# Optimization experiments

Measured on AMD Instinct MI355X. Metric: run time of the kernel, lower is better.

## Reference

```python
import jax, jax.numpy as jnp
import numpy as np

B, T, D, H, STRIDE, MLP = 2, 2048, 1024, 16, 8, 4096
HD = D // H
EPS = 1e-5


def _ln(x, g, b):
    m = x.mean(-1, keepdims=True)
    v = x.var(-1, keepdims=True)
    return (x - m) * jax.lax.rsqrt(v + EPS) * g + b


def setup_inputs() -> dict:
    key = jax.random.key(0)
    ks = jax.random.split(key, 6)
    s = lambda k, shape: (jax.random.normal(k, shape, jnp.float32) * 0.02)
    return {
        "x": jax.random.normal(ks[0], (B, T, D), jnp.float32),
        "w_in": s(ks[1], (3 * D, D)),   # torch in_proj_weight
        "b_in": jnp.zeros((3 * D,), jnp.float32),
        "w_out": s(ks[2], (D, D)),      # attn out_proj
        "b_out": jnp.zeros((D,), jnp.float32),
        "w1": s(ks[3], (MLP, D)),       # mlp first Linear (torch layout [out,in])
        "b1": jnp.zeros((MLP,), jnp.float32),
        "w2": s(ks[4], (D, MLP)),       # mlp second Linear
        "b2": jnp.zeros((D,), jnp.float32),
        "ln1_g": jnp.ones((D,), jnp.float32),
        "ln1_b": jnp.zeros((D,), jnp.float32),
        "ln2_g": jnp.ones((D,), jnp.float32),
        "ln2_b": jnp.zeros((D,), jnp.float32),
    }


def reference(x, w_in, b_in, w_out, b_out, w1, b1, w2, b2,
              ln1_g, ln1_b, ln2_g, ln2_b):
    Bs, Ts, Ds = x.shape
    xn = _ln(x, ln1_g, ln1_b)
    # fused qkv projection (torch Linear: y = x @ W.T + b)
    qkv = xn @ w_in.T + b_in                              # [B,T,3D]
    q, k, v = jnp.split(qkv, 3, axis=-1)
    to_heads = lambda t: t.reshape(Bs, Ts, H, HD).transpose(0, 2, 1, 3)
    q, k, v = to_heads(q), to_heads(k), to_heads(v)       # [B,H,T,hd]
    scores = jnp.einsum("bhqd,bhkd->bhqk", q, k) / jnp.sqrt(jnp.float32(HD))
    # mask: rows at multiples of STRIDE attend everywhere; others only to self
    idx = jnp.arange(Ts)
    allowed = ((idx % STRIDE) == 0)[:, None] | (idx[:, None] == idx[None, :])
    scores = jnp.where(allowed, scores, -jnp.inf)
    attn = jax.nn.softmax(scores, axis=-1)
    o = jnp.einsum("bhqk,bhkd->bhqd", attn, v)            # [B,H,T,hd]
    o = o.transpose(0, 2, 1, 3).reshape(Bs, Ts, Ds)
    o = o @ w_out.T + b_out
    x = x + o
    xn = _ln(x, ln2_g, ln2_b)
    h = jax.nn.gelu(xn @ w1.T + b1, approximate=False)    # torch nn.GELU default = exact
    x = x + (h @ w2.T + b2)
    return x
```

## Files before the change

### kernel.cpp

```cpp
#include <hip/hip_runtime.h>

#define D_ 1024
#define T_ 2048
#define B_ 2
#define H_ 16
#define MLP_ 4096
#define NTOK (B_*T_)
#define QG 256
#define L2E 1.44269504088896340736f

typedef float f32x4 __attribute__((ext_vector_type(4)));
typedef __bf16 bf16x8 __attribute__((ext_vector_type(8)));

__device__ __forceinline__ unsigned short f2bf(float f) {
  unsigned int u = __float_as_uint(f);
  u += 0x7fff + ((u >> 16) & 1);
  return (unsigned short)(u >> 16);
}

__device__ __forceinline__ float wave_sum(float v) {
  for (int o = 32; o > 0; o >>= 1) v += __shfl_down(v, o, 64);
  return v;
}

__device__ __forceinline__ void gload16(const unsigned short* g, unsigned short* l) {
  __builtin_amdgcn_global_load_lds(
      (const __attribute__((address_space(1))) void*)g,
      (__attribute__((address_space(3))) void*)l, 16, 0, 0);
}

__device__ __forceinline__ unsigned ldsoff(const void* p) {
  return (unsigned)(size_t)(const __attribute__((address_space(3))) void*)p;
}

__device__ __forceinline__ void agload16(const unsigned short* g, unsigned m0v) {
  unsigned su = __builtin_amdgcn_readfirstlane(m0v);
  asm volatile("s_mov_b32 m0, %0\n\t"
               "global_load_lds_dwordx4 %1, off"
               :: "s"(su), "v"(g) : "memory");
}

#define N4_WIN  786432
#define N4_WOUT 262144
#define N4_W1   1048576
#define N4_W2   1048576
#define NCASTB  12288
__global__ void castln_kernel(const float* __restrict__ w_in,
                              const float* __restrict__ w_out,
                              const float* __restrict__ w1,
                              const float* __restrict__ w2,
                              unsigned short* __restrict__ o_in,
                              unsigned short* __restrict__ o_out,
                              unsigned short* __restrict__ o1,
                              unsigned short* __restrict__ o2,
                              const float* __restrict__ x,
                              const float* __restrict__ g,
                              const float* __restrict__ b,
                              unsigned short* __restrict__ xn) {
  int blk = blockIdx.x;
  int tid = threadIdx.x;
  if (blk < NTOK) {
    int wave = tid >> 6, lane = tid & 63;
    float4 v = ((const float4*)(x + (size_t)blk * D_))[tid];
    float s  = v.x + v.y + v.z + v.w;
    float s2 = v.x*v.x + v.y*v.y + v.z*v.z + v.w*v.w;
    s = wave_sum(s); s2 = wave_sum(s2);
    __shared__ float r1[4], r2[4];
    if (lane == 0) { r1[wave] = s; r2[wave] = s2; }
    __syncthreads();
    float ts  = r1[0] + r1[1] + r1[2] + r1[3];
    float ts2 = r2[0] + r2[1] + r2[2] + r2[3];
    float mean = ts * (1.0f / D_);
    float var  = ts2 * (1.0f / D_) - mean * mean;
    float rs = rsqrtf(var + 1e-5f);
    float4 gv = ((const float4*)g)[tid];
    float4 bv = ((const float4*)b)[tid];
    ushort4 o;
    o.x = f2bf((v.x - mean) * rs * gv.x + bv.x);
    o.y = f2bf((v.y - mean) * rs * gv.y + bv.y);
    o.z = f2bf((v.z - mean) * rs * gv.z + bv.z);
    o.w = f2bf((v.w - mean) * rs * gv.w + bv.w);
    ((ushort4*)(xn + (size_t)blk * D_))[tid] = o;
  } else {
    int i = (blk - NTOK) * 256 + tid;
    const float* src; unsigned short* dst; int j = i;
    if (i < N4_WIN) { src = w_in; dst = o_in; }
    else if ((j -= N4_WIN) < N4_WOUT) { src = w_out; dst = o_out; }
    else if ((j -= N4_WOUT) < N4_W1) { src = w1; dst = o1; }
    else { j -= N4_W1; src = w2; dst = o2; }
    float4 v = ((const float4*)src)[j];
    ushort4 o;
    o.x = f2bf(v.x); o.y = f2bf(v.y); o.z = f2bf(v.z); o.w = f2bf(v.w);
    ((ushort4*)dst)[j] = o;
  }
}

__global__ void reduce_ln_kernel(const float* __restrict__ part,
                                 const float* __restrict__ x,
                                 const float* __restrict__ bias,
                                 const float* __restrict__ g,
                                 const float* __restrict__ b,
                                 float* __restrict__ x1,
                                 unsigned short* __restrict__ xn2) {
  int row = blockIdx.x;
  int tid = threadIdx.x;
  int wave = tid >> 6, lane = tid & 63;
  size_t base = (size_t)row * (D_ / 4) + tid;
  float4 v = ((const float4*)x)[base];
  float4 bo = ((const float4*)bias)[tid];
  v.x += bo.x; v.y += bo.y; v.z += bo.z; v.w += bo.w;
#pragma unroll
  for (int c = 0; c < 2; ++c) {
    float4 p = ((const float4*)part)[(size_t)c * (NTOK * (D_ / 4)) + base];
    v.x += p.x; v.y += p.y; v.z += p.z; v.w += p.w;
  }
  ((float4*)x1)[base] = v;
  float s  = v.x + v.y + v.z + v.w;
  float s2 = v.x*v.x + v.y*v.y + v.z*v.z + v.w*v.w;
  s = wave_sum(s); s2 = wave_sum(s2);
  __shared__ float r1[4], r2[4];
  if (lane == 0) { r1[wave] = s; r2[wave] = s2; }
  __syncthreads();
  float ts  = r1[0] + r1[1] + r1[2] + r1[3];
  float ts2 = r2[0] + r2[1] + r2[2] + r2[3];
  float mean = ts * (1.0f / D_);
  float var  = ts2 * (1.0f / D_) - mean * mean;
  float rs = rsqrtf(var + 1e-5f);
  float4 gv = ((const float4*)g)[tid];
  float4 bv = ((const float4*)b)[tid];
  ushort4 o;
  o.x = f2bf((v.x - mean) * rs * gv.x + bv.x);
  o.y = f2bf((v.y - mean) * rs * gv.y + bv.y);
  o.z = f2bf((v.z - mean) * rs * gv.z + bv.z);
  o.w = f2bf((v.w - mean) * rs * gv.w + bv.w);
  ((ushort4*)xn2)[base] = o;
}

__global__ void reduce_out_kernel(const float* __restrict__ part,
                                  const float* __restrict__ x1,
                                  const float* __restrict__ bias,
                                  float* __restrict__ out) {
  int i = blockIdx.x * 256 + threadIdx.x;
  float4 v = ((const float4*)x1)[i];
  float4 bo = ((const float4*)bias)[i & (D_ / 4 - 1)];
  v.x += bo.x; v.y += bo.y; v.z += bo.z; v.w += bo.w;
#pragma unroll
  for (int c = 0; c < 2; ++c) {
    float4 p = ((const float4*)part)[(size_t)c * (NTOK * (D_ / 4)) + i];
    v.x += p.x; v.y += p.y; v.z += p.z; v.w += p.w;
  }
  ((float4*)out)[i] = v;
}

template<int EPI>
__global__ __launch_bounds__(256)
void gemm128p_kernel(const unsigned short* __restrict__ A, int LDA,
                     const unsigned short* __restrict__ Bm, int LDB,
                     void* __restrict__ Cv, size_t sC, int LDC,
                     const float* __restrict__ bias,
                     int K, int nx, int ny) {
  __shared__ __align__(16) unsigned short As[2 * 8192];
  __shared__ __align__(16) unsigned short Bs[2 * 8192];
  const int flat = blockIdx.x;
  const int sxc = nx >> 1;
  const int nSuper = sxc * (ny >> 2);
  int s = flat % nSuper, pos = flat / nSuper;
  int sx = s % sxc, sy = s / sxc;
  const int bx = sx * 2 + (pos & 1);
  const int by = sy * 4 + (pos >> 1);
  const int m0 = by * 128, n0 = bx * 128;
  const int kOff = blockIdx.z * K;
  const int tid = threadIdx.x;
  const int lane = tid & 63, wave = tid >> 6;
  const int wm = (wave >> 1) * 64, wn = (wave & 1) * 64;
  const int fr = lane & 15, q = lane >> 4;
  const int f0 = ((q)     ^ (fr & 7)) << 3;
  const int f1 = ((4 + q) ^ (fr & 7)) << 3;

  const unsigned short* aS[4];
  const unsigned short* bS[4];
#pragma unroll
  for (int p = 0; p < 4; ++p) {
    int l = p * 256 + tid;
    int r = l >> 3;
    int cg = (l & 7) ^ (r & 7);
    aS[p] = A  + (size_t)(m0 + r) * LDA + kOff + cg * 8;
    bS[p] = Bm + (size_t)(n0 + r) * LDB + kOff + cg * 8;
  }
  const int NT = K >> 6;

  const unsigned aW = ldsoff(As) + wave * 1024;
  const unsigned bW = ldsoff(Bs) + wave * 1024;

#pragma unroll
  for (int p = 0; p < 4; ++p) {
    agload16(aS[p], aW + p * 4096);
    agload16(bS[p], bW + p * 4096);
  }
#pragma unroll
  for (int p = 0; p < 4; ++p) {
    agload16(aS[p] + 64, aW + 16384 + p * 4096);
    agload16(bS[p] + 64, bW + 16384 + p * 4096);
  }
  asm volatile("s_waitcnt vmcnt(8)");
  __builtin_amdgcn_sched_barrier(0);
  __builtin_amdgcn_s_barrier();

  f32x4 acc[4][4] = {};
  for (int t = 0; t < NT; ++t) {
    const int cb = (t & 1) << 13;
    const unsigned cbB = (t & 1) << 14;
    const unsigned short* Ab = As + cb;
    const unsigned short* Bb = Bs + cb;
    const int ko2 = (t + 2) << 6;
    {
      bf16x8 af[4], bfr[4];
#pragma unroll
      for (int i = 0; i < 4; ++i) af[i]  = *(const bf16x8*)&Ab[(wm + i * 16 + fr) * 64 + f0];
#pragma unroll
      for (int j = 0; j < 4; ++j) bfr[j] = *(const bf16x8*)&Bb[(wn + j * 16 + fr) * 64 + f0];
#pragma unroll
      for (int i = 0; i < 4; ++i)
#pragma unroll
        for (int j = 0; j < 4; ++j)
          acc[i][j] = __builtin_amdgcn_mfma_f32_16x16x32_bf16(af[i], bfr[j], acc[i][j], 0, 0, 0);
    }
    {
      bf16x8 af[4], bfr[4];
#pragma unroll
      for (int i = 0; i < 4; ++i) af[i]  = *(const bf16x8*)&Ab[(wm + i * 16 + fr) * 64 + f1];
#pragma unroll
      for (int j = 0; j < 4; ++j) bfr[j] = *(const bf16x8*)&Bb[(wn + j * 16 + fr) * 64 + f1];
#pragma unroll
      for (int i = 0; i < 4; ++i)
#pragma unroll
        for (int j = 0; j < 4; ++j)
          acc[i][j] = __builtin_amdgcn_mfma_f32_16x16x32_bf16(af[i], bfr[j], acc[i][j], 0, 0, 0);
    }
    __builtin_amdgcn_s_barrier();
    if (t + 2 < NT) {
#pragma unroll
      for (int p = 0; p < 4; ++p) {
        agload16(aS[p] + ko2, aW + cbB + p * 4096);
        agload16(bS[p] + ko2, bW + cbB + p * 4096);
      }
    }
    if (t + 1 < NT) {
      if (t + 2 < NT) asm volatile("s_waitcnt vmcnt(8)");
      else            asm volatile("s_waitcnt vmcnt(0)");
      __builtin_amdgcn_sched_barrier(0);
    }
    __builtin_amdgcn_s_barrier();
  }

  const int col = lane & 15, rbase = (lane >> 4) * 4;
#pragma unroll
  for (int i = 0; i < 4; ++i) {
#pragma unroll
    for (int j = 0; j < 4; ++j) {
      int gn = n0 + wn + j * 16 + col;
      int gmb = m0 + wm + i * 16 + rbase;
      float bv = (EPI == 2) ? bias[gn] : 0.0f;
#pragma unroll
      for (int r = 0; r < 4; ++r) {
        int gm = gmb + r;
        float v = acc[i][j][r] + bv;
        if (EPI == 2) {
          float u = v * (1.5957691216f + 0.0713548162f * v * v);
          float gl = v / (1.0f + exp2f(-L2E * u));
          ((unsigned short*)Cv)[(size_t)gm * LDC + gn] = f2bf(gl);
        } else {
          ((float*)Cv)[(size_t)blockIdx.z * sC + (size_t)gm * LDC + gn] = v;
        }
      }
    }
  }
}

template<int EPI>
__global__ __launch_bounds__(512)
void gemm256a_kernel(const unsigned short* __restrict__ A, int LDA,
                     const unsigned short* __restrict__ Bm, int LDB,
                     void* __restrict__ Cv, size_t sC, int LDC,
                     const float* __restrict__ bias,
                     int K, int nx) {
  __shared__ __align__(16) unsigned short As[2 * 16384];
  __shared__ __align__(16) unsigned short Bs[2 * 16384];
  const int tid = threadIdx.x;
  const int lane = tid & 63, w = tid >> 6;
  const int wm = w >> 2, wn = w & 3;
  const int fr = lane & 15, q = lane >> 4, xr = fr & 7;

  const int nwg = gridDim.x;
  const int bid = blockIdx.x;
  const int l = (bid & 7) * (nwg >> 3) + (bid >> 3);
  const int bx = l % nx, by = l / nx;
  const int m0 = by * 256, n0 = bx * 256;
  const int kOff = blockIdx.z * K;

  const unsigned short* aS[4];
  const unsigned short* bS[4];
#pragma unroll
  for (int s = 0; s < 4; ++s) {
    int ls = s * 512 + tid;
    int r = ls >> 3;
    int cg = (ls & 7) ^ (r & 7);
    aS[s] = A  + (size_t)(m0 + r) * LDA + kOff + cg * 8;
    bS[s] = Bm + (size_t)(n0 + r) * LDB + kOff + cg * 8;
  }
  const int NT = K >> 6;

  const unsigned asb = ldsoff(As), bsb = ldsoff(Bs);
  const unsigned aW = asb + w * 1024, bW = bsb + w * 1024;

#pragma unroll
  for (int s = 0; s < 4; ++s) {
    agload16(aS[s], aW + s * 8192);
    agload16(bS[s], bW + s * 8192);
  }
#pragma unroll
  for (int s = 0; s < 4; ++s) {
    agload16(aS[s] + 64, aW + 32768 + s * 8192);
    agload16(bS[s] + 64, bW + 32768 + s * 8192);
  }
  asm volatile("s_waitcnt vmcnt(8)");
  __builtin_amdgcn_sched_barrier(0);
  __builtin_amdgcn_s_barrier();

  const int aOff = ((wm * 128 + fr) << 7) + ((q ^ xr) << 4);
  const int bOff = ((wn * 64 + fr) << 7) + ((q ^ xr) << 4);

  f32x4 acc[8][4] = {};

  for (int t = 0; t < NT; ++t) {
    const int cb = (t & 1) << 15;
    const char* Ab = (const char*)As + cb;
    const char* Bb = (const char*)Bs + cb;
    const unsigned aWc = aW + cb, bWc = bW + cb;
    const int ko2 = (t + 2) << 6;
    bf16x8 af[2][4], bfr[2][4];

#pragma unroll
    for (int i = 0; i < 4; ++i) {
      af[0][i] = *(const bf16x8*)(Ab + aOff + i * 2048);
      af[1][i] = *(const bf16x8*)(Ab + (aOff ^ 64) + i * 2048);
    }
#pragma unroll
    for (int j = 0; j < 2; ++j) {
      bfr[0][j] = *(const bf16x8*)(Bb + bOff + j * 2048);
      bfr[1][j] = *(const bf16x8*)(Bb + (bOff ^ 64) + j * 2048);
    }
    __builtin_amdgcn_s_barrier();
    __builtin_amdgcn_s_setprio(1);
#pragma unroll
    for (int i = 0; i < 4; ++i)
#pragma unroll
      for (int j = 0; j < 2; ++j) {
        acc[i][j] = __builtin_amdgcn_mfma_f32_16x16x32_bf16(af[0][i], bfr[0][j], acc[i][j], 0, 0, 0);
        acc[i][j] = __builtin_amdgcn_mfma_f32_16x16x32_bf16(af[1][i], bfr[1][j], acc[i][j], 0, 0, 0);
      }
    __builtin_amdgcn_s_setprio(0);
    __builtin_amdgcn_s_barrier();

#pragma unroll
    for (int j = 2; j < 4; ++j) {
      bfr[0][j] = *(const bf16x8*)(Bb + bOff + j * 2048);
      bfr[1][j] = *(const bf16x8*)(Bb + (bOff ^ 64) + j * 2048);
    }
    if (t + 2 < NT) {
      agload16(aS[0] + ko2, aWc);
      agload16(aS[2] + ko2, aWc + 16384);
    }
    __builtin_amdgcn_s_barrier();
    __builtin_amdgcn_s_setprio(1);
#pragma unroll
    for (int i = 0; i < 4; ++i)
#pragma unroll
      for (int j = 0; j < 2; ++j) {
        acc[i][2 + j] = __builtin_amdgcn_mfma_f32_16x16x32_bf16(af[0][i], bfr[0][2 + j], acc[i][2 + j], 0, 0, 0);
        acc[i][2 + j] = __builtin_amdgcn_mfma_f32_16x16x32_bf16(af[1][i], bfr[1][2 + j], acc[i][2 + j], 0, 0, 0);
      }
    __builtin_amdgcn_s_setprio(0);
    __builtin_amdgcn_s_barrier();

#pragma unroll
    for (int i = 0; i < 4; ++i) {
      af[0][i] = *(const bf16x8*)(Ab + (aOff + 8192) + i * 2048);
      af[1][i] = *(const bf16x8*)(Ab + ((aOff + 8192) ^ 64) + i * 2048);
    }
    if (t + 2 < NT) {
      agload16(bS[0] + ko2, bWc);
      agload16(bS[1] + ko2, bWc + 8192);
      agload16(bS[2] + ko2, bWc + 16384);
      agload16(bS[3] + ko2, bWc + 24576);
    }
    __builtin_amdgcn_s_barrier();
    __builtin_amdgcn_s_setprio(1);
#pragma unroll
    for (int i = 0; i < 4; ++i)
#pragma unroll
      for (int j = 0; j < 2; ++j) {
        acc[4 + i][j] = __builtin_amdgcn_mfma_f32_16x16x32_bf16(af[0][i], bfr[0][j], acc[4 + i][j], 0, 0, 0);
        acc[4 + i][j] = __builtin_amdgcn_mfma_f32_16x16x32_bf16(af[1][i], bfr[1][j], acc[4 + i][j], 0, 0, 0);
      }
    __builtin_amdgcn_s_setprio(0);
    __builtin_amdgcn_s_barrier();

    if (t + 2 < NT) {
      agload16(aS[1] + ko2, aWc + 8192);
      agload16(aS[3] + ko2, aWc + 24576);
    }
    if (t + 1 < NT) {
      if (t + 2 < NT) asm volatile("s_waitcnt vmcnt(8)");
      else            asm volatile("s_waitcnt vmcnt(0)");
      __builtin_amdgcn_sched_barrier(0);
    }
    __builtin_amdgcn_s_barrier();
    __builtin_amdgcn_s_setprio(1);
#pragma unroll
    for (int i = 0; i < 4; ++i)
#pragma unroll
      for (int j = 0; j < 2; ++j) {
        acc[4 + i][2 + j] = __builtin_amdgcn_mfma_f32_16x16x32_bf16(af[0][i], bfr[0][2 + j], acc[4 + i][2 + j], 0, 0, 0);
        acc[4 + i][2 + j] = __builtin_amdgcn_mfma_f32_16x16x32_bf16(af[1][i], bfr[1][2 + j], acc[4 + i][2 + j], 0, 0, 0);
      }
    __builtin_amdgcn_s_setprio(0);
    __builtin_amdgcn_s_barrier();
  }

  const int col = lane & 15, rbase = (lane >> 4) * 4;
  const int gm0 = m0 + wm * 128 + rbase;
  const int gn0 = n0 + wn * 64 + col;
#pragma unroll
  for (int mi = 0; mi < 8; ++mi) {
#pragma unroll
    for (int j = 0; j < 4; ++j) {
      int gn = gn0 + j * 16;
      float bv = (EPI == 2) ? bias[gn] : 0.0f;
#pragma unroll
      for (int r = 0; r < 4; ++r) {
        int gm = gm0 + mi * 16 + r;
        float v = acc[mi][j][r] + bv;
        if (EPI == 2) {
          float u = v * (1.5957691216f + 0.0713548162f * v * v);
          float gl = v / (1.0f + exp2f(-L2E * u));
          ((unsigned short*)Cv)[(size_t)gm * LDC + gn] = f2bf(gl);
        } else {
          ((float*)Cv)[(size_t)blockIdx.z * sC + (size_t)gm * LDC + gn] = v;
        }
      }
    }
  }
}

template<int EPI>
__global__ __launch_bounds__(512)
void gemm256b_kernel(const unsigned short* __restrict__ A, int LDA,
                     const unsigned short* __restrict__ Bm, int LDB,
                     unsigned short* __restrict__ Cv, int LDC,
                     const float* __restrict__ bias,
                     unsigned short* __restrict__ aux1,
                     unsigned short* __restrict__ aux2,
                     int K, int nx) {
  __shared__ __align__(16) unsigned short As[2 * 4096];
  __shared__ __align__(16) unsigned short Bs[2 * 8192];
  const int tid = threadIdx.x;
  const int lane = tid & 63, wv = tid >> 6;
  const int wm = (wv >> 2) * 64, wn = (wv & 3) * 64;
  const int fr = lane & 15, q = lane >> 4;

  const int nwg = gridDim.x;
  const int bid = blockIdx.x;
  const int l = (bid & 7) * (nwg >> 3) + (bid >> 3);
  const int bx = l % nx, by = l / nx;
  const int m0 = by * 128, n0 = bx * 256;

  const int rA = tid >> 2, sA = tid & 3;
  const int cA = sA ^ ((rA >> 1) & 3);
  const unsigned short* aSrc = A  + (size_t)(m0 + rA) * LDA + cA * 8;
  const unsigned short* bSrc0 = Bm + (size_t)(n0 + rA) * LDB + cA * 8;
  const unsigned short* bSrc1 = Bm + (size_t)(n0 + 128 + rA) * LDB + cA * 8;
  const int NT = K >> 5;

  const unsigned aWb = ldsoff(As) + wv * 1024;
  const unsigned bWb = ldsoff(Bs) + wv * 1024;

  agload16(aSrc, aWb);
  agload16(bSrc0, bWb);
  agload16(bSrc1, bWb + 8192);
  agload16(aSrc + 32, aWb + 8192);
  agload16(bSrc0 + 32, bWb + 16384);
  agload16(bSrc1 + 32, bWb + 24576);
  asm volatile("s_waitcnt vmcnt(3)");
  __builtin_amdgcn_sched_barrier(0);
  __builtin_amdgcn_s_barrier();

  f32x4 acc[4][4] = {};
  for (int t = 0; t < NT; ++t) {
    const unsigned cbA = (t & 1) ? 8192u : 0u;
    const unsigned cbB = (t & 1) ? 16384u : 0u;
    const char* Ab = (const char*)As + cbA;
    const char* Bb = (const char*)Bs + cbB;
    const int ko2 = (t + 2) << 5;
    bf16x8 af[4], bfr[4];
#pragma unroll
    for (int i = 0; i < 4; ++i) {
      int ra = wm + i * 16 + fr;
      af[i] = *(const bf16x8*)(Ab + ra * 64 + ((q ^ ((ra >> 1) & 3)) << 4));
    }
#pragma unroll
    for (int j = 0; j < 4; ++j) {
      int rb = wn + j * 16 + fr;
      bfr[j] = *(const bf16x8*)(Bb + rb * 64 + ((q ^ ((rb >> 1) & 3)) << 4));
    }
#pragma unroll
    for (int i = 0; i < 4; ++i)
#pragma unroll
      for (int j = 0; j < 4; ++j)
        acc[i][j] = __builtin_amdgcn_mfma_f32_16x16x32_bf16(af[i], bfr[j], acc[i][j], 0, 0, 0);
    __builtin_amdgcn_s_barrier();
    if (t + 2 < NT) {
      agload16(aSrc + ko2, aWb + cbA);
      agload16(bSrc0 + ko2, bWb + cbB);
      agload16(bSrc1 + ko2, bWb + cbB + 8192);
    }
    if (t + 1 < NT) {
      if (t + 2 < NT) asm volatile("s_waitcnt vmcnt(3)");
      else            asm volatile("s_waitcnt vmcnt(0)");
      __builtin_amdgcn_sched_barrier(0);
    }
    __builtin_amdgcn_s_barrier();
  }

  const int col = lane & 15, rbase = (lane >> 4) * 4;
#pragma unroll
  for (int i = 0; i < 4; ++i) {
#pragma unroll
    for (int j = 0; j < 4; ++j) {
      int gn = n0 + wn + j * 16 + col;
      int gmb = m0 + wm + i * 16 + rbase;
      float bv = bias[gn];
#pragma unroll
      for (int r = 0; r < 4; ++r) {
        int gm = gmb + r;
        float v = acc[i][j][r] + bv;
        if (EPI == 2) {
          float u = v * (1.5957691216f + 0.0713548162f * v * v);
          float gl = v / (1.0f + exp2f(-L2E * u));
          Cv[(size_t)gm * LDC + gn] = f2bf(gl);
        } else {
          int sec = gn >> 10;
          int hh = (gn >> 6) & (H_ - 1);
          int dd = gn & 63;
          int t = gm & (T_ - 1);
          int b = gm >> 11;
          unsigned short bf = f2bf(v);
          if (sec == 0) {
            if (!(t & 7))
              aux1[(((size_t)(b * H_ + hh)) * QG + (t >> 3)) * 64 + dd] = bf;
          } else if (sec == 1) {
            aux2[(((size_t)(b * H_ + hh)) * T_ + t) * 64 + dd] = bf;
          } else {
            Cv[(size_t)gm * D_ + (gn - 2 * D_)] = bf;
          }
        }
      }
    }
  }
}

__global__ void vtrans_kernel(const unsigned short* __restrict__ vcomp,
                              unsigned short* __restrict__ Vt) {
  int blk = blockIdx.x;
  int tchunk = blk & 31;
  int bh = blk >> 5;
  int h = bh & (H_ - 1), b = bh >> 4;
  int t0 = tchunk * 64;
  __shared__ unsigned short ls[64][66];
  int tid = threadIdx.x;
#pragma unroll
  for (int it = 0; it < 16; ++it) {
    int linear = it * 256 + tid;
    int d = linear & 63, tl = linear >> 6;
    ls[d][tl] = vcomp[((size_t)(b * T_ + t0 + tl)) * D_ + h * 64 + d];
  }
  __syncthreads();
#pragma unroll
  for (int it = 0; it < 16; ++it) {
    int linear = it * 256 + tid;
    int tl = linear & 63, d = linear >> 6;
    Vt[((size_t)(bh * 64 + d)) * T_ + t0 + tl] = ls[d][tl];
  }
}

__global__ __launch_bounds__(256)
void flash_kernel(const unsigned short* __restrict__ Qg,
                  const unsigned short* __restrict__ Kh,
                  const unsigned short* __restrict__ Vt,
                  float* __restrict__ Opart,
                  float* __restrict__ ml) {
  const int kc = blockIdx.x, qt = blockIdx.y, bh = blockIdx.z;
  const int tid = threadIdx.x;
  const int lane = tid & 63, w = tid >> 6;
  const int fr = lane & 15, quad = lane >> 4;

  __shared__ __align__(16) unsigned short Qs[64 * 64];
  __shared__ __align__(16) unsigned short Ks[128 * 64];
  __shared__ __align__(16) unsigned short Vs[64 * 128];
  __shared__ __align__(16) unsigned short Ps[4 * 16 * 128];

  const unsigned short* Qbase = Qg + ((size_t)bh * 256 + qt * 64) * 64;
#pragma unroll
  for (int p = 0; p < 2; ++p) {
    int linear = p * 256 + tid;
    int r = linear >> 3, c = linear & 7;
    gload16(Qbase + r * 64 + (c ^ (r & 7)) * 8, &Qs[linear * 8]);
  }

  float m_run[4], l_run[4];
  f32x4 O[4] = {};
#pragma unroll
  for (int r = 0; r < 4; ++r) { m_run[r] = -3.0e38f; l_run[r] = 0.f; }

  const unsigned short* Kc = Kh + ((size_t)bh * T_ + kc * 512) * 64;
  const unsigned short* Vc = Vt + (size_t)bh * 64 * T_ + kc * 512;
  unsigned short* Pw = &Ps[w * 2048];
  const int arow = w * 16 + fr;

  for (int kt = 0; kt < 4; ++kt) {
    __syncthreads();
#pragma unroll
    for (int p = 0; p < 4; ++p) {
      int linear = p * 256 + tid;
      int r = linear >> 3, c = linear & 7;
      gload16(Kc + (size_t)(kt * 128 + r) * 64 + (c ^ (r & 7)) * 8, &Ks[linear * 8]);
    }
#pragma unroll
    for (int p = 0; p < 4; ++p) {
      int linear = p * 256 + tid;
      int r = linear >> 4, c = linear & 15;
      gload16(Vc + (size_t)r * T_ + kt * 128 + (c ^ (r & 7)) * 8, &Vs[linear * 8]);
    }
    __syncthreads();

    f32x4 s[8] = {};
    bf16x8 aq[2];
#pragma unroll
    for (int ks = 0; ks < 2; ++ks)
      aq[ks] = *(const bf16x8*)&Qs[arow * 64 + ((ks * 4 + quad) ^ (fr & 7)) * 8];
#pragma unroll
    for (int nf = 0; nf < 8; ++nf) {
      int krow = nf * 16 + fr;
#pragma unroll
      for (int ks = 0; ks < 2; ++ks) {
        bf16x8 bk = *(const bf16x8*)&Ks[krow * 64 + ((ks * 4 + quad) ^ (fr & 7)) * 8];
        s[nf] = __builtin_amdgcn_mfma_f32_16x16x32_bf16(aq[ks], bk, s[nf], 0, 0, 0);
      }
    }
    float alpha[4], rowsum[4];
#pragma unroll
    for (int r = 0; r < 4; ++r) {
      float mt = -3.0e38f;
#pragma unroll
      for (int nf = 0; nf < 8; ++nf) { s[nf][r] *= 0.125f; mt = fmaxf(mt, s[nf][r]); }
#pragma unroll
      for (int x = 1; x < 16; x <<= 1) mt = fmaxf(mt, __shfl_xor(mt, x, 64));
      float mn = fmaxf(m_run[r], mt);
      alpha[r] = exp2f((m_run[r] - mn) * L2E);
      m_run[r] = mn;
      rowsum[r] = 0.f;
    }
#pragma unroll
    for (int nf = 0; nf < 8; ++nf)
#pragma unroll
      for (int r = 0; r < 4; ++r) {
        float p = exp2f((s[nf][r] - m_run[r]) * L2E);
        s[nf][r] = p; rowsum[r] += p;
      }
#pragma unroll
    for (int r = 0; r < 4; ++r) {
#pragma unroll
      for (int x = 1; x < 16; x <<= 1) rowsum[r] += __shfl_xor(rowsum[r], x, 64);
      l_run[r] = l_run[r] * alpha[r] + rowsum[r];
    }
#pragma unroll
    for (int nf = 0; nf < 8; ++nf)
#pragma unroll
      for (int r = 0; r < 4; ++r) {
        int m = quad * 4 + r;
        int c = nf * 2 + (fr >> 3);
        Pw[m * 128 + ((c ^ (m & 7)) * 8) + (fr & 7)] = f2bf(s[nf][r]);
      }
#pragma unroll
    for (int nf2 = 0; nf2 < 4; ++nf2)
#pragma unroll
      for (int r = 0; r < 4; ++r) O[nf2][r] *= alpha[r];
#pragma unroll
    for (int ks2 = 0; ks2 < 4; ++ks2) {
      bf16x8 ap = *(const bf16x8*)&Pw[fr * 128 + (((ks2 * 4 + quad) ^ (fr & 7)) * 8)];
#pragma unroll
      for (int nf2 = 0; nf2 < 4; ++nf2) {
        int vrow = nf2 * 16 + fr;
        bf16x8 bv = *(const bf16x8*)&Vs[vrow * 128 + (((ks2 * 4 + quad) ^ (fr & 7)) * 8)];
        O[nf2] = __builtin_amdgcn_mfma_f32_16x16x32_bf16(ap, bv, O[nf2], 0, 0, 0);
      }
    }
  }

  int qbase = qt * 64 + w * 16;
  float* Ob = Opart + (((size_t)bh * 4 + kc) * 256 + qbase) * 64;
#pragma unroll
  for (int nf2 = 0; nf2 < 4; ++nf2)
#pragma unroll
    for (int r = 0; r < 4; ++r)
      Ob[(size_t)(quad * 4 + r) * 64 + nf2 * 16 + fr] = O[nf2][r];
  if (fr == 0) {
#pragma unroll
    for (int r = 0; r < 4; ++r) {
      size_t mi = ((((size_t)bh * 4 + kc) * 256) + qbase + quad * 4 + r) * 2;
      ml[mi] = m_run[r]; ml[mi + 1] = l_run[r];
    }
  }
}

__global__ void combine_kernel(const float* __restrict__ Opart,
                               const float* __restrict__ ml,
                               unsigned short* __restrict__ vcomp) {
  int idx = blockIdx.x * 256 + threadIdx.x;
  int c = idx & (D_ - 1);
  int qi = (idx >> 10) & (QG - 1);
  int b = idx >> 18;
  int h = c >> 6, d = c & 63;
  int bh = b * H_ + h;
  float m[4], l[4];
  float M = -3.0e38f;
#pragma unroll
  for (int ch = 0; ch < 4; ++ch) {
    size_t r = ((size_t)bh * 4 + ch) * 256 + qi;
    m[ch] = ml[r * 2]; l[ch] = ml[r * 2 + 1];
    M = fmaxf(M, m[ch]);
  }
  float osum = 0.f, lsum = 0.f;
#pragma unroll
  for (int ch = 0; ch < 4; ++ch) {
    size_t r = ((size_t)bh * 4 + ch) * 256 + qi;
    float wgt = exp2f((m[ch] - M) * L2E);
    osum += wgt * Opart[r * 64 + d];
    lsum += wgt * l[ch];
  }
  vcomp[((size_t)(b * T_ + qi * 8)) * D_ + c] = f2bf(osum / lsum);
}

extern "C" void kernel_launch(void* const* d_in, const int* in_sizes, int n_in,
                              void* d_out, int out_size, void* d_ws, size_t ws_size,
                              hipStream_t stream) {
  const float* x     = (const float*)d_in[0];
  const float* w_in  = (const float*)d_in[1];
  const float* b_in  = (const float*)d_in[2];
  const float* w_out = (const float*)d_in[3];
  const float* b_out = (const float*)d_in[4];
  const float* w1    = (const float*)d_in[5];
  const float* b1    = (const float*)d_in[6];
  const float* w2    = (const float*)d_in[7];
  const float* b2    = (const float*)d_in[8];
  const float* ln1_g = (const float*)d_in[9];
  const float* ln1_b = (const float*)d_in[10];
  const float* ln2_g = (const float*)d_in[11];
  const float* ln2_b = (const float*)d_in[12];
  float* out = (float*)d_out;

  char* ws = (char*)d_ws;
  size_t off = 0;
  auto alloc = [&](size_t bytes) -> void* {
    void* p = ws + off;
    off += (bytes + 255) & ~(size_t)255;
    return p;
  };
  unsigned short* w_inb = (unsigned short*)alloc((size_t)3 * D_ * D_ * 2);
  unsigned short* w_outb= (unsigned short*)alloc((size_t)D_ * D_ * 2);
  unsigned short* w1b   = (unsigned short*)alloc((size_t)MLP_ * D_ * 2);
  unsigned short* w2b   = (unsigned short*)alloc((size_t)D_ * MLP_ * 2);
  unsigned short* vcomp = (unsigned short*)alloc((size_t)NTOK * D_ * 2);
  float*          x1    = (float*)         alloc((size_t)NTOK * D_ * 4);
  unsigned short* xn2   = (unsigned short*)alloc((size_t)NTOK * D_ * 2);
  unsigned short* h     = (unsigned short*)alloc((size_t)NTOK * MLP_ * 2);
  char* U = (char*)alloc((size_t)40 * 1024 * 1024);
  float*          P2    = (float*)U;
  unsigned short* xn    = (unsigned short*)U;
  unsigned short* Qg    = (unsigned short*)(U + 8388608);
  unsigned short* Kh    = (unsigned short*)(U + 12582912);
  unsigned short* Vt    = (unsigned short*)(U + 20971520);
  float*          Opart = (float*)         (U + 29360128);
  float*          mlbuf = (float*)         (U + 37748736);

  castln_kernel<<<NTOK + NCASTB, 256, 0, stream>>>(
      w_in, w_out, w1, w2, w_inb, w_outb, w1b, w2b, x, ln1_g, ln1_b, xn);

  gemm256b_kernel<8><<<dim3(384, 1, 1), 512, 0, stream>>>(
      xn, D_, w_inb, D_, vcomp, 3 * D_, b_in, Qg, Kh, 1024, 12);

  vtrans_kernel<<<1024, 256, 0, stream>>>(vcomp, Vt);

  flash_kernel<<<dim3(4, 4, 32), 256, 0, stream>>>(Qg, Kh, Vt, Opart, mlbuf);

  combine_kernel<<<2048, 256, 0, stream>>>(Opart, mlbuf, vcomp);

  gemm128p_kernel<7><<<dim3(8 * 32, 1, 2), 256, 0, stream>>>(
      vcomp, D_, w_outb, D_, P2, (size_t)NTOK * D_, D_, nullptr,
      512, 8, 32);

  reduce_ln_kernel<<<NTOK, 256, 0, stream>>>(P2, x, b_out, ln2_g, ln2_b, x1, xn2);

  gemm256a_kernel<2><<<dim3(256, 1, 1), 512, 0, stream>>>(
      xn2, D_, w1b, D_, h, 0, MLP_, b1, 1024, 16);

  gemm128p_kernel<7><<<dim3(8 * 32, 1, 2), 256, 0, stream>>>(
      h, MLP_, w2b, MLP_, P2, (size_t)NTOK * D_, D_, nullptr,
      2048, 8, 32);

  reduce_out_kernel<<<4096, 256, 0, stream>>>(P2, x1, b2, out);
}
```

Measured before the change: 314.2 us.

## Replace split-K GEMMs with 64x128 tile GEMM fusing bias and residual

The out-projection and MLP-down GEMMs no longer use split-K with two partial fp32 buffers followed by separate reduction kernels. They now use a 64x128 tile GEMM over the full K dimension, with 512 blocks in an XCD-interleaved order, and add bias and residual directly in the epilogue. This removes the partial-sum writes and reads and the extra reduce launch. The cost is longer K loops per block, since the MLP-down GEMM now runs all 4096 of K in one block, and lower arithmetic intensity per tile.

```diff
diff --git a/kernel.cpp b/kernel.cpp
--- a/kernel.cpp
+++ b/kernel.cpp
@@ -95,26 +95,12 @@
   }
 }
 
-__global__ void reduce_ln_kernel(const float* __restrict__ part,
-                                 const float* __restrict__ x,
-                                 const float* __restrict__ bias,
-                                 const float* __restrict__ g,
-                                 const float* __restrict__ b,
-                                 float* __restrict__ x1,
-                                 unsigned short* __restrict__ xn2) {
+__global__ void ln_kernel(const float* __restrict__ x, const float* __restrict__ g,
+                          const float* __restrict__ b, unsigned short* __restrict__ out) {
   int row = blockIdx.x;
   int tid = threadIdx.x;
   int wave = tid >> 6, lane = tid & 63;
-  size_t base = (size_t)row * (D_ / 4) + tid;
-  float4 v = ((const float4*)x)[base];
-  float4 bo = ((const float4*)bias)[tid];
-  v.x += bo.x; v.y += bo.y; v.z += bo.z; v.w += bo.w;
-#pragma unroll
-  for (int c = 0; c < 2; ++c) {
-    float4 p = ((const float4*)part)[(size_t)c * (NTOK * (D_ / 4)) + base];
-    v.x += p.x; v.y += p.y; v.z += p.z; v.w += p.w;
-  }
-  ((float4*)x1)[base] = v;
+  float4 v = ((const float4*)(x + (size_t)row * D_))[tid];
   float s  = v.x + v.y + v.z + v.w;
   float s2 = v.x*v.x + v.y*v.y + v.z*v.z + v.w*v.w;
   s = wave_sum(s); s2 = wave_sum(s2);
@@ -133,59 +119,46 @@
   o.y = f2bf((v.y - mean) * rs * gv.y + bv.y);
   o.z = f2bf((v.z - mean) * rs * gv.z + bv.z);
   o.w = f2bf((v.w - mean) * rs * gv.w + bv.w);
-  ((ushort4*)xn2)[base] = o;
-}
-
-__global__ void reduce_out_kernel(const float* __restrict__ part,
-                                  const float* __restrict__ x1,
-                                  const float* __restrict__ bias,
-                                  float* __restrict__ out) {
-  int i = blockIdx.x * 256 + threadIdx.x;
-  float4 v = ((const float4*)x1)[i];
-  float4 bo = ((const float4*)bias)[i & (D_ / 4 - 1)];
-  v.x += bo.x; v.y += bo.y; v.z += bo.z; v.w += bo.w;
-#pragma unroll
-  for (int c = 0; c < 2; ++c) {
-    float4 p = ((const float4*)part)[(size_t)c * (NTOK * (D_ / 4)) + i];
-    v.x += p.x; v.y += p.y; v.z += p.z; v.w += p.w;
-  }
-  ((float4*)out)[i] = v;
-}
-
-template<int EPI>
+  ((ushort4*)(out + (size_t)row * D_))[tid] = o;
+}
+
 __global__ __launch_bounds__(256)
-void gemm128p_kernel(const unsigned short* __restrict__ A, int LDA,
-                     const unsigned short* __restrict__ Bm, int LDB,
-                     void* __restrict__ Cv, size_t sC, int LDC,
-                     const float* __restrict__ bias,
-                     int K, int nx, int ny) {
-  __shared__ __align__(16) unsigned short As[2 * 8192];
+void gemm64p_kernel(const unsigned short* __restrict__ A, int LDA,
+                    const unsigned short* __restrict__ Bm, int LDB,
+                    float* __restrict__ C,
+                    const float* __restrict__ bias,
+                    const float* __restrict__ xres,
+                    int K, int nx) {
+  __shared__ __align__(16) unsigned short As[2 * 4096];
   __shared__ __align__(16) unsigned short Bs[2 * 8192];
-  const int flat = blockIdx.x;
-  const int sxc = nx >> 1;
-  const int nSuper = sxc * (ny >> 2);
-  int s = flat % nSuper, pos = flat / nSuper;
-  int sx = s % sxc, sy = s / sxc;
-  const int bx = sx * 2 + (pos & 1);
-  const int by = sy * 4 + (pos >> 1);
-  const int m0 = by * 128, n0 = bx * 128;
-  const int kOff = blockIdx.z * K;
   const int tid = threadIdx.x;
   const int lane = tid & 63, wave = tid >> 6;
-  const int wm = (wave >> 1) * 64, wn = (wave & 1) * 64;
+  const int wm = (wave >> 1) * 32, wn = (wave & 1) * 64;
   const int fr = lane & 15, q = lane >> 4;
   const int f0 = ((q)     ^ (fr & 7)) << 3;
   const int f1 = ((4 + q) ^ (fr & 7)) << 3;
 
-  const unsigned short* aS[4];
+  const int nwg = gridDim.x;
+  const int bid = blockIdx.x;
+  const int l = (bid & 7) * (nwg >> 3) + (bid >> 3);
+  const int bx = l % nx, by = l / nx;
+  const int m0 = by * 64, n0 = bx * 128;
+
+  const unsigned short* aS[2];
   const unsigned short* bS[4];
 #pragma unroll
+  for (int p = 0; p < 2; ++p) {
+    int ls = p * 256 + tid;
+    int r = ls >> 3;
+    int cg = (ls & 7) ^ (r & 7);
+    aS[p] = A + (size_t)(m0 + r) * LDA + cg * 8;
+  }
+#pragma unroll
   for (int p = 0; p < 4; ++p) {
-    int l = p * 256 + tid;
-    int r = l >> 3;
-    int cg = (l & 7) ^ (r & 7);
-    aS[p] = A  + (size_t)(m0 + r) * LDA + kOff + cg * 8;
-    bS[p] = Bm + (size_t)(n0 + r) * LDB + kOff + cg * 8;
+    int ls = p * 256 + tid;
+    int r = ls >> 3;
+    int cg = (ls & 7) ^ (r & 7);
+    bS[p] = Bm + (size_t)(n0 + r) * LDB + cg * 8;
   }
   const int NT = K >> 6;
 
@@ -193,46 +166,46 @@
   const unsigned bW = ldsoff(Bs) + wave * 1024;
 
 #pragma unroll
-  for (int p = 0; p < 4; ++p) {
-    agload16(aS[p], aW + p * 4096);
-    agload16(bS[p], bW + p * 4096);
-  }
-#pragma unroll
-  for (int p = 0; p < 4; ++p) {
-    agload16(aS[p] + 64, aW + 16384 + p * 4096);
-    agload16(bS[p] + 64, bW + 16384 + p * 4096);
-  }
-  asm volatile("s_waitcnt vmcnt(8)");
+  for (int p = 0; p < 2; ++p) agload16(aS[p], aW + p * 4096);
+#pragma unroll
+  for (int p = 0; p < 4; ++p) agload16(bS[p], bW + p * 4096);
+#pragma unroll
+  for (int p = 0; p < 2; ++p) agload16(aS[p] + 64, aW + 8192 + p * 4096);
+#pragma unroll
+  for (int p = 0; p < 4; ++p) agload16(bS[p] + 64, bW + 16384 + p * 4096);
+  asm volatile("s_waitcnt vmcnt(6)");
   __builtin_amdgcn_sched_barrier(0);
   __builtin_amdgcn_s_barrier();
 
-  f32x4 acc[4][4] = {};
+  f32x4 acc[2][4] = {};
   for (int t = 0; t < NT; ++t) {
-    const int cb = (t & 1) << 13;
-    const unsigned cbB = (t & 1) << 14;
-    const unsigned short* Ab = As + cb;
-    const unsigned short* Bb = Bs + cb;
+    const int cbA = (t & 1) << 12;
+    const int cbB = (t & 1) << 13;
+    const unsigned cbAB = (t & 1) << 13;
+    const unsigned cbBB = (t & 1) << 14;
+    const unsigned short* Ab = As + cbA;
+    const unsigned short* Bb = Bs + cbB;
     const int ko2 = (t + 2) << 6;
     {
-      bf16x8 af[4], bfr[4];
-#pragma unroll
-      for (int i = 0; i < 4; ++i) af[i]  = *(const bf16x8*)&Ab[(wm + i * 16 + fr) * 64 + f0];
+      bf16x8 af[2], bfr[4];
+#pragma unroll
+      for (int i = 0; i < 2; ++i) af[i]  = *(const bf16x8*)&Ab[(wm + i * 16 + fr) * 64 + f0];
 #pragma unroll
       for (int j = 0; j < 4; ++j) bfr[j] = *(const bf16x8*)&Bb[(wn + j * 16 + fr) * 64 + f0];
 #pragma unroll
-      for (int i = 0; i < 4; ++i)
+      for (int i = 0; i < 2; ++i)
 #pragma unroll
         for (int j = 0; j < 4; ++j)
           acc[i][j] = __builtin_amdgcn_mfma_f32_16x16x32_bf16(af[i], bfr[j], acc[i][j], 0, 0, 0);
     }
     {
-      bf16x8 af[4], bfr[4];
-#pragma unroll
-      for (int i = 0; i < 4; ++i) af[i]  = *(const bf16x8*)&Ab[(wm + i * 16 + fr) * 64 + f1];
+      bf16x8 af[2], bfr[4];
+#pragma unroll
+      for (int i = 0; i < 2; ++i) af[i]  = *(const bf16x8*)&Ab[(wm + i * 16 + fr) * 64 + f1];
 #pragma unroll
       for (int j = 0; j < 4; ++j) bfr[j] = *(const bf16x8*)&Bb[(wn + j * 16 + fr) * 64 + f1];
 #pragma unroll
-      for (int i = 0; i < 4; ++i)
+      for (int i = 0; i < 2; ++i)
 #pragma unroll
         for (int j = 0; j < 4; ++j)
           acc[i][j] = __builtin_amdgcn_mfma_f32_16x16x32_bf16(af[i], bfr[j], acc[i][j], 0, 0, 0);
@@ -240,13 +213,12 @@
     __builtin_amdgcn_s_barrier();
     if (t + 2 < NT) {
 #pragma unroll
-      for (int p = 0; p < 4; ++p) {
-        agload16(aS[p] + ko2, aW + cbB + p * 4096);
-        agload16(bS[p] + ko2, bW + cbB + p * 4096);
-      }
+      for (int p = 0; p < 2; ++p) agload16(aS[p] + ko2, aW + cbAB + p * 4096);
+#pragma unroll
+      for (int p = 0; p < 4; ++p) agload16(bS[p] + ko2, bW + cbBB + p * 4096);
     }
     if (t + 1 < NT) {
-      if (t + 2 < NT) asm volatile("s_waitcnt vmcnt(8)");
+      if (t + 2 < NT) asm volatile("s_waitcnt vmcnt(6)");
       else            asm volatile("s_waitcnt vmcnt(0)");
       __builtin_amdgcn_sched_barrier(0);
     }
@@ -255,23 +227,17 @@
 
   const int col = lane & 15, rbase = (lane >> 4) * 4;
 #pragma unroll
-  for (int i = 0; i < 4; ++i) {
+  for (int i = 0; i < 2; ++i) {
 #pragma unroll
     for (int j = 0; j < 4; ++j) {
       int gn = n0 + wn + j * 16 + col;
       int gmb = m0 + wm + i * 16 + rbase;
-      float bv = (EPI == 2) ? bias[gn] : 0.0f;
+      float bv = bias[gn];
 #pragma unroll
       for (int r = 0; r < 4; ++r) {
         int gm = gmb + r;
-        float v = acc[i][j][r] + bv;
-        if (EPI == 2) {
-          float u = v * (1.5957691216f + 0.0713548162f * v * v);
-          float gl = v / (1.0f + exp2f(-L2E * u));
-          ((unsigned short*)Cv)[(size_t)gm * LDC + gn] = f2bf(gl);
-        } else {
-          ((float*)Cv)[(size_t)blockIdx.z * sC + (size_t)gm * LDC + gn] = v;
-        }
+        size_t idx = (size_t)gm * D_ + gn;
+        C[idx] = acc[i][j][r] + bv + xres[idx];
       }
     }
   }
@@ -785,7 +751,6 @@
   unsigned short* xn2   = (unsigned short*)alloc((size_t)NTOK * D_ * 2);
   unsigned short* h     = (unsigned short*)alloc((size_t)NTOK * MLP_ * 2);
   char* U = (char*)alloc((size_t)40 * 1024 * 1024);
-  float*          P2    = (float*)U;
   unsigned short* xn    = (unsigned short*)U;
   unsigned short* Qg    = (unsigned short*)(U + 8388608);
   unsigned short* Kh    = (unsigned short*)(U + 12582912);
@@ -805,18 +770,14 @@
 
   combine_kernel<<<2048, 256, 0, stream>>>(Opart, mlbuf, vcomp);
 
-  gemm128p_kernel<7><<<dim3(8 * 32, 1, 2), 256, 0, stream>>>(
-      vcomp, D_, w_outb, D_, P2, (size_t)NTOK * D_, D_, nullptr,
-      512, 8, 32);
-
-  reduce_ln_kernel<<<NTOK, 256, 0, stream>>>(P2, x, b_out, ln2_g, ln2_b, x1, xn2);
+  gemm64p_kernel<<<dim3(512, 1, 1), 256, 0, stream>>>(
+      vcomp, D_, w_outb, D_, x1, b_out, x, 1024, 8);
+
+  ln_kernel<<<NTOK, 256, 0, stream>>>(x1, ln2_g, ln2_b, xn2);
 
   gemm256a_kernel<2><<<dim3(256, 1, 1), 512, 0, stream>>>(
       xn2, D_, w1b, D_, h, 0, MLP_, b1, 1024, 16);
 
-  gemm128p_kernel<7><<<dim3(8 * 32, 1, 2), 256, 0, stream>>>(
-      h, MLP_, w2b, MLP_, P2, (size_t)NTOK * D_, D_, nullptr,
-      2048, 8, 32);
-
-  reduce_out_kernel<<<4096, 256, 0, stream>>>(P2, x1, b2, out);
-}
+  gemm64p_kernel<<<dim3(512, 1, 1), 256, 0, stream>>>(
+      h, MLP_, w2b, MLP_, out, b2, x1, 4096, 8);
+}
```

Result: faster. 294.0 us (-6.4%).
